# Performance work log

Measured on AMD Instinct MI355X. Metric: run time of the kernel, lower is better.

Reference implementation:

```python
import jax, jax.numpy as jnp
import numpy as np

N_NODES = 100000


def graph_conv(x, src, dst, Wr, br, Wroot):
    # PyG GraphConv (aggr='add'): out_i = W_rel @ sum_{j in N(i)} x_j + b_rel + W_root @ x_i
    msgs = x[src]                                              # [E, F] gather
    agg = jax.ops.segment_sum(msgs, dst, num_segments=N_NODES)  # [N, F] scatter-add
    return agg @ Wr + br + x @ Wroot


def setup_inputs() -> dict:
    key = jax.random.key(0)
    k1, k2, k3, k4 = jax.random.split(key, 4)
    F = 128
    E = 600000
    x = jax.random.normal(k1, (N_NODES, F), dtype=jnp.float32)
    edge_index = jax.random.randint(k2, (2, E), 0, N_NODES, dtype=jnp.int64)
    scale = 1.0 / np.sqrt(F)
    W_rel = jax.random.normal(k3, (5, F, F), dtype=jnp.float32) * scale
    b_rel = jnp.zeros((5, F), dtype=jnp.float32)
    W_root = jax.random.normal(k4, (5, F, F), dtype=jnp.float32) * scale
    return {"x": x, "edge_index": edge_index, "W_rel": W_rel, "b_rel": b_rel, "W_root": W_root}


def reference(x, edge_index, W_rel, b_rel, W_root):
    src, dst = edge_index[0], edge_index[1]
    x1 = jax.nn.relu(graph_conv(x, src, dst, W_rel[0], b_rel[0], W_root[0]))
    x2 = jax.nn.relu(graph_conv(x1, src, dst, W_rel[1], b_rel[1], W_root[1])) + x1
    x3 = jax.nn.relu(graph_conv(x2, src, dst, W_rel[2], b_rel[2], W_root[2])) + x2
    x4 = jax.nn.relu(graph_conv(x3, src, dst, W_rel[3], b_rel[3], W_root[3])) + x3
    x5 = graph_conv(x4, src, dst, W_rel[4], b_rel[4], W_root[4]) + x4
    return x5
```

## Files before the change

### kernel.cpp

```cpp
#include <hip/hip_runtime.h>

#define NNODES 100000
#define FDIM 128
#define NLAYERS 5

typedef __bf16 bf16_t;
typedef bf16_t bf16x8 __attribute__((ext_vector_type(8)));
typedef float  f32x4  __attribute__((ext_vector_type(4)));

__device__ __forceinline__ bf16_t f2bf(float f){ return (bf16_t)f; }
__device__ __forceinline__ float bfbits_lo(unsigned u){
  unsigned b = u << 16; return __builtin_bit_cast(float, b);
}
__device__ __forceinline__ float bfbits_hi(unsigned u){
  unsigned b = u & 0xffff0000u; return __builtin_bit_cast(float, b);
}
__device__ __forceinline__ unsigned short bfb(float f){
  bf16_t b = (bf16_t)f; return __builtin_bit_cast(unsigned short, b);
}
__device__ __forceinline__ float us2f(unsigned short u){
  unsigned b = ((unsigned)u) << 16; return __builtin_bit_cast(float, b);
}

__global__ void deg_kernel(const int* __restrict__ dstv, int* __restrict__ deg, int E){
  int e = blockIdx.x*256 + threadIdx.x;
  if(e < E) atomicAdd(&deg[dstv[e]], 1);
}

__global__ void scan1_kernel(const int* __restrict__ deg, int* __restrict__ row_start,
                             int* __restrict__ sums, int n){
  __shared__ int sm[256];
  int t = threadIdx.x;
  int base = blockIdx.x*1024 + t*4;
  int v0=0,v1=0,v2=0,v3=0;
  if(base+3 < n){ int4 q = *(const int4*)(deg+base); v0=q.x; v1=q.y; v2=q.z; v3=q.w; }
  else {
    if(base   < n) v0 = deg[base];
    if(base+1 < n) v1 = deg[base+1];
    if(base+2 < n) v2 = deg[base+2];
    if(base+3 < n) v3 = deg[base+3];
  }
  int s = v0+v1+v2+v3;
  sm[t] = s;
  __syncthreads();
  for(int off=1; off<256; off<<=1){
    int y = (t>=off) ? sm[t-off] : 0;
    __syncthreads();
    sm[t] += y;
    __syncthreads();
  }
  int excl = sm[t] - s;
  if(base   < n) row_start[base]   = excl;
  if(base+1 < n) row_start[base+1] = excl+v0;
  if(base+2 < n) row_start[base+2] = excl+v0+v1;
  if(base+3 < n) row_start[base+3] = excl+v0+v1+v2;
  if(t == 255) sums[blockIdx.x] = sm[255];
}

__global__ void scan2_kernel(int* sums, int nc){
  __shared__ int sm[128];
  int t = threadIdx.x;
  int v = (t<nc) ? sums[t] : 0;
  sm[t] = v;
  __syncthreads();
  for(int off=1; off<128; off<<=1){
    int y = (t>=off) ? sm[t-off] : 0;
    __syncthreads();
    sm[t] += y;
    __syncthreads();
  }
  if(t<nc) sums[t] = sm[t] - v;
}

__global__ void scan3_kernel(int* row_start, const int* __restrict__ sums, int n, int E){
  int i = blockIdx.x*256 + threadIdx.x;
  if(i < n)       row_start[i] += sums[i>>10];
  else if(i == n) row_start[n]  = E;
}

__global__ void fill_kernel(const int* __restrict__ srcv, const int* __restrict__ dstv,
                            const int* __restrict__ row_start, int* __restrict__ cnt,
                            int* __restrict__ csr, int E){
  int e = blockIdx.x*256 + threadIdx.x;
  if(e < E){
    int d = dstv[e];
    int p = atomicAdd(&cnt[d], 1);
    csr[row_start[d] + p] = srcv[e];
  }
}

__global__ __launch_bounds__(256) void cvt_kernel(const float* __restrict__ x,
                                                  unsigned short* __restrict__ xb){
  long i = ((long)blockIdx.x*256 + threadIdx.x)*8;
  float4 q0 = *(const float4*)(x+i);
  float4 q1 = *(const float4*)(x+i+4);
  unsigned short o[8];
  o[0]=bfb(q0.x); o[1]=bfb(q0.y); o[2]=bfb(q0.z); o[3]=bfb(q0.w);
  o[4]=bfb(q1.x); o[5]=bfb(q1.y); o[6]=bfb(q1.z); o[7]=bfb(q1.w);
  *(ulong2*)(xb+i) = *(ulong2*)o;
}

__global__ __launch_bounds__(256) void gather_kernel(const unsigned short* __restrict__ xb,
                                                     const int* __restrict__ row_start,
                                                     const int* __restrict__ csr,
                                                     unsigned short* __restrict__ agg, int n){
  int wid  = (blockIdx.x*256 + threadIdx.x) >> 6;
  int lane = threadIdx.x & 63;
  if(wid >= n) return;
  int s0 = row_start[wid];
  int s1 = row_start[wid+1];
  float ax[8] = {}, ay[8] = {};
  int i = s0;
  for(; i+8 <= s1; i += 8){
    unsigned v[8];
    #pragma unroll
    for(int j=0;j<8;j++){
      int c = csr[i+j];
      v[j] = *(const unsigned*)(xb + (size_t)c*FDIM + lane*2);
    }
    #pragma unroll
    for(int j=0;j<8;j++){ ax[j] += bfbits_lo(v[j]); ay[j] += bfbits_hi(v[j]); }
  }
  if(i+4 <= s1){
    unsigned v[4];
    #pragma unroll
    for(int j=0;j<4;j++){
      int c = csr[i+j];
      v[j] = *(const unsigned*)(xb + (size_t)c*FDIM + lane*2);
    }
    #pragma unroll
    for(int j=0;j<4;j++){ ax[j] += bfbits_lo(v[j]); ay[j] += bfbits_hi(v[j]); }
    i += 4;
  }
  if(i+2 <= s1){
    unsigned v0 = *(const unsigned*)(xb + (size_t)csr[i]*FDIM + lane*2);
    unsigned v1 = *(const unsigned*)(xb + (size_t)csr[i+1]*FDIM + lane*2);
    ax[4] += bfbits_lo(v0); ay[4] += bfbits_hi(v0);
    ax[5] += bfbits_lo(v1); ay[5] += bfbits_hi(v1);
    i += 2;
  }
  if(i < s1){
    unsigned v0 = *(const unsigned*)(xb + (size_t)csr[i]*FDIM + lane*2);
    ax[6] += bfbits_lo(v0); ay[6] += bfbits_hi(v0);
  }
  float axs = ((ax[0]+ax[1])+(ax[2]+ax[3])) + ((ax[4]+ax[5])+(ax[6]+ax[7]));
  float ays = ((ay[0]+ay[1])+(ay[2]+ay[3])) + ((ay[4]+ay[5])+(ay[6]+ay[7]));
  unsigned o = (unsigned)bfb(axs) | ((unsigned)bfb(ays) << 16);
  *(unsigned*)(agg + (size_t)wid*FDIM + lane*2) = o;
}

__global__ void wprep_kernel(const float* __restrict__ Wrel, const float* __restrict__ Wroot,
                             bf16_t* __restrict__ Bp){
  int gid = blockIdx.x*256 + threadIdx.x;
  if(gid >= NLAYERS*64*64) return;
  int lane = gid & 63;
  int fg   = (gid>>6) & 63;
  int l    = gid >> 12;
  int kk = fg >> 3, cb = fg & 7;
  int kbase = kk*32 + (lane>>4)*8;
  int col   = cb*16 + (lane&15);
  bf16_t tmp[8];
  #pragma unroll
  for(int e=0;e<8;e++){
    int k = kbase + e;
    float v = (k < FDIM) ? Wrel [l*FDIM*FDIM + k*FDIM + col]
                         : Wroot[l*FDIM*FDIM + (k-FDIM)*FDIM + col];
    tmp[e] = f2bf(v);
  }
  bf16_t* o = Bp + (long)gid*8;
  #pragma unroll
  for(int e=0;e<8;e++) o[e] = tmp[e];
}

__global__ __launch_bounds__(256, 1) void gemm_kernel(
    const bf16_t* __restrict__ Aagg, const bf16_t* __restrict__ Ain,
    const bf16_t* __restrict__ Bp, const float* __restrict__ bias,
    bf16_t* __restrict__ outB, float* __restrict__ outF,
    int relu, int resf, int npairs){
  int lane = threadIdx.x & 63;
  int gw   = (blockIdx.x*256 + threadIdx.x) >> 6;
  if(gw >= npairs) return;
  int r_lo = lane & 15;
  int kgrp = lane >> 4;
  long r0 = (long)gw*32;

  const bf16_t* pa0 = Aagg + (r0      + r_lo)*FDIM + kgrp*8;
  const bf16_t* pa1 = Aagg + (r0 + 16 + r_lo)*FDIM + kgrp*8;
  const bf16_t* pi0 = Ain  + (r0      + r_lo)*FDIM + kgrp*8;
  const bf16_t* pi1 = Ain  + (r0 + 16 + r_lo)*FDIM + kgrp*8;

  bf16x8 wcur[8], wnxt[8];
  #pragma unroll
  for(int cb=0;cb<8;cb++) wcur[cb] = *(const bf16x8*)(Bp + (cb*64 + lane)*8);

  f32x4 acc0[8] = {};
  f32x4 acc1[8] = {};
  #pragma unroll
  for(int kk=0;kk<8;kk++){
    bf16x8 a0 = (kk<4) ? *(const bf16x8*)(pa0 + kk*32) : *(const bf16x8*)(pi0 + (kk-4)*32);
    bf16x8 a1 = (kk<4) ? *(const bf16x8*)(pa1 + kk*32) : *(const bf16x8*)(pi1 + (kk-4)*32);
    if(kk < 7){
      #pragma unroll
      for(int cb=0;cb<8;cb++)
        wnxt[cb] = *(const bf16x8*)(Bp + ((((kk+1)<<3)|cb)*64 + lane)*8);
    }
    #pragma unroll
    for(int cb=0;cb<8;cb++){
      acc0[cb] = __builtin_amdgcn_mfma_f32_16x16x32_bf16(wcur[cb], a0, acc0[cb], 0, 0, 0);
      acc1[cb] = __builtin_amdgcn_mfma_f32_16x16x32_bf16(wcur[cb], a1, acc1[cb], 0, 0, 0);
    }
    if(kk < 7){
      #pragma unroll
      for(int cb=0;cb<8;cb++) wcur[cb] = wnxt[cb];
    }
  }
  #pragma unroll
  for(int half=0; half<2; half++){
    long nrow = r0 + half*16 + r_lo;
    f32x4* acc = half ? acc1 : acc0;
    #pragma unroll
    for(int cb=0;cb<8;cb++){
      int col = cb*16 + kgrp*4;
      float4 bv = *(const float4*)(bias + col);
      float v0 = acc[cb][0] + bv.x;
      float v1 = acc[cb][1] + bv.y;
      float v2 = acc[cb][2] + bv.z;
      float v3 = acc[cb][3] + bv.w;
      if(relu){ v0=fmaxf(v0,0.f); v1=fmaxf(v1,0.f); v2=fmaxf(v2,0.f); v3=fmaxf(v3,0.f); }
      if(resf){
        ushort4 rv = *(const ushort4*)((const unsigned short*)Ain + nrow*FDIM + col);
        v0 += us2f(rv.x); v1 += us2f(rv.y); v2 += us2f(rv.z); v3 += us2f(rv.w);
      }
      if(outF){
        float4 o; o.x=v0; o.y=v1; o.z=v2; o.w=v3;
        *(float4*)(outF + nrow*FDIM + col) = o;
      } else {
        uint2 o;
        o.x = (unsigned)bfb(v0) | ((unsigned)bfb(v1) << 16);
        o.y = (unsigned)bfb(v2) | ((unsigned)bfb(v3) << 16);
        *(uint2*)((unsigned short*)outB + nrow*FDIM + col) = o;
      }
    }
  }
}

extern "C" void kernel_launch(void* const* d_in, const int* in_sizes, int n_in,
                              void* d_out, int out_size, void* d_ws, size_t ws_size,
                              hipStream_t stream){
  const float* x     = (const float*)d_in[0];
  const int*   ei    = (const int*)  d_in[1];
  const float* Wrel  = (const float*)d_in[2];
  const float* brel  = (const float*)d_in[3];
  const float* Wroot = (const float*)d_in[4];
  float* out = (float*)d_out;

  const int N = NNODES;
  const int E = in_sizes[1] / 2;
  const int* srcv = ei;
  const int* dstv = ei + E;

  char* w = (char*)d_ws;
  auto alloc = [&](size_t b)->char*{ char* p = w; w += (b + 255) & ~(size_t)255; return p; };
  unsigned short* xb  = (unsigned short*)alloc((size_t)N*FDIM*2);
  unsigned short* h_a = (unsigned short*)alloc((size_t)N*FDIM*2);
  unsigned short* h_b = (unsigned short*)alloc((size_t)N*FDIM*2);
  unsigned short* agg = (unsigned short*)alloc((size_t)N*FDIM*2);
  int*    deg       = (int*)   alloc((size_t)N*4);
  int*    cnt       = (int*)   alloc((size_t)N*4);
  int*    row_start = (int*)   alloc((size_t)(N+1)*4);
  int*    csr       = (int*)   alloc((size_t)E*4);
  bf16_t* Bp        = (bf16_t*)alloc((size_t)NLAYERS*4096*8*2);
  int*    sums      = (int*)   alloc(512);

  hipMemsetAsync(deg, 0, (size_t)N*4, stream);
  hipMemsetAsync(cnt, 0, (size_t)N*4, stream);

  int eb = (E + 255) / 256;
  int nchunks = (N + 1023) / 1024;
  deg_kernel <<<eb, 256, 0, stream>>>(dstv, deg, E);
  scan1_kernel<<<nchunks, 256, 0, stream>>>(deg, row_start, sums, N);
  scan2_kernel<<<1, 128, 0, stream>>>(sums, nchunks);
  scan3_kernel<<<(N + 1 + 255)/256, 256, 0, stream>>>(row_start, sums, N, E);
  fill_kernel<<<eb, 256, 0, stream>>>(srcv, dstv, row_start, cnt, csr, E);
  wprep_kernel<<<(NLAYERS*4096 + 255)/256, 256, 0, stream>>>(Wrel, Wroot, Bp);
  cvt_kernel  <<<(N*FDIM/8 + 255)/256, 256, 0, stream>>>(x, xb);

  const int npairs  = N / 32;
  const int gblocks = (npairs + 3) / 4;

  typedef unsigned short us;
  struct Lay { const us* in; us* o; int relu; int res; };
  Lay L[5] = {
    { xb,  h_a, 1, 0 },
    { h_a, h_b, 1, 1 },
    { h_b, h_a, 1, 1 },
    { h_a, h_b, 1, 1 },
    { h_b, 0,   0, 1 },
  };
  for(int l=0; l<NLAYERS; l++){
    gather_kernel<<<N/4, 256, 0, stream>>>(L[l].in, row_start, csr, agg, N);
    gemm_kernel  <<<gblocks, 256, 0, stream>>>((const bf16_t*)agg, (const bf16_t*)L[l].in,
                                               Bp + (size_t)l*4096*8,
                                               brel + l*FDIM,
                                               (bf16_t*)L[l].o, (l==4)? out : nullptr,
                                               L[l].relu, L[l].res, npairs);
  }
}
```

Measured before the change: 447.3 us.

## Shrink GEMM wave tile to 16 rows and drop weight double-buffering

Each wave now computes a 16-row output tile instead of 32 rows. Weight fragments are loaded directly inside the MFMA loop rather than through a register double buffer, and the single-block launch-bounds restriction is removed. The aim is to cut register pressure and double the number of waves, for better latency hiding and occupancy. In exchange, each loaded weight fragment is reused half as much, which raises weight traffic from cache.

```diff
diff --git a/kernel.cpp b/kernel.cpp
--- a/kernel.cpp
+++ b/kernel.cpp
@@ -172,74 +172,53 @@
   for(int e=0;e<8;e++) o[e] = tmp[e];
 }
 
-__global__ __launch_bounds__(256, 1) void gemm_kernel(
+__global__ __launch_bounds__(256) void gemm_kernel(
     const bf16_t* __restrict__ Aagg, const bf16_t* __restrict__ Ain,
     const bf16_t* __restrict__ Bp, const float* __restrict__ bias,
     bf16_t* __restrict__ outB, float* __restrict__ outF,
-    int relu, int resf, int npairs){
+    int relu, int resf, int ntiles){
   int lane = threadIdx.x & 63;
-  int gw   = (blockIdx.x*256 + threadIdx.x) >> 6;
-  if(gw >= npairs) return;
+  int t    = (blockIdx.x*256 + threadIdx.x) >> 6;
+  if(t >= ntiles) return;
   int r_lo = lane & 15;
   int kgrp = lane >> 4;
-  long r0 = (long)gw*32;
-
-  const bf16_t* pa0 = Aagg + (r0      + r_lo)*FDIM + kgrp*8;
-  const bf16_t* pa1 = Aagg + (r0 + 16 + r_lo)*FDIM + kgrp*8;
-  const bf16_t* pi0 = Ain  + (r0      + r_lo)*FDIM + kgrp*8;
-  const bf16_t* pi1 = Ain  + (r0 + 16 + r_lo)*FDIM + kgrp*8;
-
-  bf16x8 wcur[8], wnxt[8];
-  #pragma unroll
-  for(int cb=0;cb<8;cb++) wcur[cb] = *(const bf16x8*)(Bp + (cb*64 + lane)*8);
-
-  f32x4 acc0[8] = {};
-  f32x4 acc1[8] = {};
+  long r0 = (long)t*16;
+
+  const bf16_t* pa = Aagg + (r0 + r_lo)*FDIM + kgrp*8;
+  const bf16_t* pi = Ain  + (r0 + r_lo)*FDIM + kgrp*8;
+
+  f32x4 acc[8] = {};
   #pragma unroll
   for(int kk=0;kk<8;kk++){
-    bf16x8 a0 = (kk<4) ? *(const bf16x8*)(pa0 + kk*32) : *(const bf16x8*)(pi0 + (kk-4)*32);
-    bf16x8 a1 = (kk<4) ? *(const bf16x8*)(pa1 + kk*32) : *(const bf16x8*)(pi1 + (kk-4)*32);
-    if(kk < 7){
-      #pragma unroll
-      for(int cb=0;cb<8;cb++)
-        wnxt[cb] = *(const bf16x8*)(Bp + ((((kk+1)<<3)|cb)*64 + lane)*8);
-    }
+    bf16x8 a = (kk<4) ? *(const bf16x8*)(pa + kk*32) : *(const bf16x8*)(pi + (kk-4)*32);
     #pragma unroll
     for(int cb=0;cb<8;cb++){
-      acc0[cb] = __builtin_amdgcn_mfma_f32_16x16x32_bf16(wcur[cb], a0, acc0[cb], 0, 0, 0);
-      acc1[cb] = __builtin_amdgcn_mfma_f32_16x16x32_bf16(wcur[cb], a1, acc1[cb], 0, 0, 0);
-    }
-    if(kk < 7){
-      #pragma unroll
-      for(int cb=0;cb<8;cb++) wcur[cb] = wnxt[cb];
-    }
-  }
-  #pragma unroll
-  for(int half=0; half<2; half++){
-    long nrow = r0 + half*16 + r_lo;
-    f32x4* acc = half ? acc1 : acc0;
-    #pragma unroll
-    for(int cb=0;cb<8;cb++){
-      int col = cb*16 + kgrp*4;
-      float4 bv = *(const float4*)(bias + col);
-      float v0 = acc[cb][0] + bv.x;
-      float v1 = acc[cb][1] + bv.y;
-      float v2 = acc[cb][2] + bv.z;
-      float v3 = acc[cb][3] + bv.w;
-      if(relu){ v0=fmaxf(v0,0.f); v1=fmaxf(v1,0.f); v2=fmaxf(v2,0.f); v3=fmaxf(v3,0.f); }
-      if(resf){
-        ushort4 rv = *(const ushort4*)((const unsigned short*)Ain + nrow*FDIM + col);
-        v0 += us2f(rv.x); v1 += us2f(rv.y); v2 += us2f(rv.z); v3 += us2f(rv.w);
-      }
-      if(outF){
-        float4 o; o.x=v0; o.y=v1; o.z=v2; o.w=v3;
-        *(float4*)(outF + nrow*FDIM + col) = o;
-      } else {
-        uint2 o;
-        o.x = (unsigned)bfb(v0) | ((unsigned)bfb(v1) << 16);
-        o.y = (unsigned)bfb(v2) | ((unsigned)bfb(v3) << 16);
-        *(uint2*)((unsigned short*)outB + nrow*FDIM + col) = o;
-      }
+      bf16x8 wfr = *(const bf16x8*)(Bp + (((kk<<3)|cb)*64 + lane)*8);
+      acc[cb] = __builtin_amdgcn_mfma_f32_16x16x32_bf16(wfr, a, acc[cb], 0, 0, 0);
+    }
+  }
+  long nrow = r0 + r_lo;
+  #pragma unroll
+  for(int cb=0;cb<8;cb++){
+    int col = cb*16 + kgrp*4;
+    float4 bv = *(const float4*)(bias + col);
+    float v0 = acc[cb][0] + bv.x;
+    float v1 = acc[cb][1] + bv.y;
+    float v2 = acc[cb][2] + bv.z;
+    float v3 = acc[cb][3] + bv.w;
+    if(relu){ v0=fmaxf(v0,0.f); v1=fmaxf(v1,0.f); v2=fmaxf(v2,0.f); v3=fmaxf(v3,0.f); }
+    if(resf){
+      ushort4 rv = *(const ushort4*)((const unsigned short*)Ain + nrow*FDIM + col);
+      v0 += us2f(rv.x); v1 += us2f(rv.y); v2 += us2f(rv.z); v3 += us2f(rv.w);
+    }
+    if(outF){
+      float4 o; o.x=v0; o.y=v1; o.z=v2; o.w=v3;
+      *(float4*)(outF + nrow*FDIM + col) = o;
+    } else {
+      uint2 o;
+      o.x = (unsigned)bfb(v0) | ((unsigned)bfb(v1) << 16);
+      o.y = (unsigned)bfb(v2) | ((unsigned)bfb(v3) << 16);
+      *(uint2*)((unsigned short*)outB + nrow*FDIM + col) = o;
     }
   }
 }
@@ -285,8 +264,8 @@
   wprep_kernel<<<(NLAYERS*4096 + 255)/256, 256, 0, stream>>>(Wrel, Wroot, Bp);
   cvt_kernel  <<<(N*FDIM/8 + 255)/256, 256, 0, stream>>>(x, xb);
 
-  const int npairs  = N / 32;
-  const int gblocks = (npairs + 3) / 4;
+  const int ntiles  = N / 16;
+  const int gblocks = (ntiles + 3) / 4;
 
   typedef unsigned short us;
   struct Lay { const us* in; us* o; int relu; int res; };
@@ -303,6 +282,6 @@
                                                Bp + (size_t)l*4096*8,
                                                brel + l*FDIM,
                                                (bf16_t*)L[l].o, (l==4)? out : nullptr,
-                                               L[l].relu, L[l].res, npairs);
-  }
-}
+                                               L[l].relu, L[l].res, ntiles);
+  }
+}
```

Result: faster. 429.5 us (-4.0%).
